# Optimization experiments

Hardware: AMD Instinct MI355X
Metric: run time of the kernel (lower is better)

## Reference

```python
import jax, jax.numpy as jnp
import numpy as np

HID = 2048      # hidden_size
NH = 32         # num query heads
NKV = 8         # num kv heads
HD = HID // NH  # head_dim = 64
E = 4           # num_experts
N = 2048        # flattened token count (divisible by E)
THETA = 10000.0
EPS = 1e-6


def setup_inputs() -> dict:
    key = jax.random.key(0)
    ks = jax.random.split(key, 8)
    s = HID ** -0.5
    return {
        "hidden_states": jax.random.normal(ks[0], (N, HID), jnp.float32),
        "positions": jnp.arange(N, dtype=jnp.int32),
        "sort_idx": jax.random.permutation(ks[1], N).astype(jnp.int32),
        "q_proj_w": jax.random.normal(ks[2], (E, HID, NH * HD), jnp.float32) * s,
        "o_proj_w": jax.random.normal(ks[3], (E, NH * HD, HID), jnp.float32) * s,
        "k_w": jax.random.normal(ks[4], (HID, NKV * HD), jnp.float32) * s,
        "v_w": jax.random.normal(ks[5], (HID, NKV * HD), jnp.float32) * s,
        "q_norm_w": jnp.ones((HD,), jnp.float32),
        "k_norm_w": jnp.ones((HD,), jnp.float32),
    }


def _routed_proj(x, weight, sort_idx):
    # x: [N, din], weight: [E, din, dout], sort_idx: permutation of N
    n, din = x.shape
    e, _, dout = weight.shape
    chunk = n // e
    sorted_x = x[sort_idx].reshape(e, chunk, din)          # gather + split
    sorted_out = jnp.einsum('ecd,edo->eco', sorted_x, weight).reshape(n, dout)
    return jnp.zeros((n, dout), sorted_out.dtype).at[sort_idx].set(sorted_out)


def _rms_norm(x, w):
    # x: [N, H, D] normalized over last dim
    var = jnp.mean(jnp.square(x), axis=-1, keepdims=True)
    return x * jax.lax.rsqrt(var + EPS) * w


def _rope_neox(x, positions):
    # x: [N, H, D]
    half = HD // 2
    inv_freq = 1.0 / (THETA ** (jnp.arange(0, HD, 2, dtype=jnp.float32) / HD))  # [D/2]
    freqs = positions.astype(jnp.float32)[:, None] * inv_freq                   # [N, D/2]
    cos = jnp.cos(freqs)[:, None, :]  # [N,1,D/2]
    sin = jnp.sin(freqs)[:, None, :]
    x1, x2 = x[..., :half], x[..., half:]
    return jnp.concatenate([x1 * cos - x2 * sin, x2 * cos + x1 * sin], axis=-1)


def reference(hidden_states, positions, sort_idx, q_proj_w, o_proj_w, k_w, v_w,
              q_norm_w, k_norm_w):
    n = hidden_states.shape[0]
    # projections
    q = _routed_proj(hidden_states, q_proj_w, sort_idx)        # [N, NH*HD]
    k = hidden_states @ k_w                                    # [N, NKV*HD]
    v = hidden_states @ v_w                                    # [N, NKV*HD]
    # qk norm per head
    q = _rms_norm(q.reshape(n, NH, HD), q_norm_w)
    k = _rms_norm(k.reshape(n, NKV, HD), k_norm_w)
    # rotary (neox style)
    q = _rope_neox(q, positions)
    k = _rope_neox(k, positions)
    v = v.reshape(n, NKV, HD)
    # GQA causal attention over the packed sequence
    g = NH // NKV
    k_rep = jnp.repeat(k, g, axis=1)  # [N, NH, HD]
    v_rep = jnp.repeat(v, g, axis=1)
    scores = jnp.einsum('qhd,khd->hqk', q, k_rep) * (HD ** -0.5)
    causal = positions[:, None] >= positions[None, :]          # [N, N]
    scores = jnp.where(causal[None], scores, jnp.finfo(scores.dtype).min)
    attn = jax.nn.softmax(scores, axis=-1)
    o = jnp.einsum('hqk,khd->qhd', attn, v_rep).reshape(n, NH * HD)
    # routed output projection
    return _routed_proj(o, o_proj_w, sort_idx)
```

## Files before the change

### kernel.cpp

```cpp
#include <hip/hip_runtime.h>
#include <hip/hip_bf16.h>

#define N_TOK 2048
#define HID   2048
#define NH    32
#define NKV   8
#define HD    64
#define NEXP  4
#define CHUNK (N_TOK / NEXP)

typedef __attribute__((ext_vector_type(8))) short short8;
typedef __attribute__((ext_vector_type(4))) short short4v;
typedef __attribute__((ext_vector_type(4))) float float4v;

#define QSCALE (0.125f * 1.44269504f)
#define RLOG   0.41524101186f

__device__ inline short f2bf(float f) {
    __hip_bfloat16 h = __float2bfloat16(f);
    return *reinterpret_cast<short*>(&h);
}
__device__ inline float bf2f(short s) {
    __hip_bfloat16 h = *reinterpret_cast<__hip_bfloat16*>(&s);
    return __bfloat162float(h);
}
__device__ __forceinline__ float fast_exp2(float x) {
    float r;
    asm("v_exp_f32 %0, %1" : "=v"(r) : "v"(x));
    return r;
}

__device__ __forceinline__ void gld_lds16(const void* g, void* l) {
    __builtin_amdgcn_global_load_lds(
        (const __attribute__((address_space(1))) unsigned int*)g,
        (__attribute__((address_space(3))) unsigned int*)l, 16, 0, 0);
}

__device__ __forceinline__ void wtrans_tile(
    const float* __restrict__ in, short* __restrict__ out, int Nw,
    int k0, int n0, float (*T)[65], int t)
{
    const int nl4 = (t & 15) * 4;
    const int kl  = t >> 4;
#pragma unroll
    for (int i = 0; i < 4; i++) {
        float4 v = *(const float4*)&in[(size_t)(k0 + kl + i * 16) * Nw + n0 + nl4];
        float* Tr = &T[kl + i * 16][nl4];
        Tr[0] = v.x; Tr[1] = v.y; Tr[2] = v.z; Tr[3] = v.w;
    }
    __syncthreads();
#pragma unroll
    for (int i = 0; i < 2; i++) {
        int idx = t + i * 256;
        int nl = idx >> 3, k8 = (idx & 7) * 8;
        short8 s;
#pragma unroll
        for (int j = 0; j < 8; j++) s[j] = f2bf(T[k8 + j][nl]);
        *(short8*)&out[(size_t)(n0 + nl) * 2048 + k0 + k8] = s;
    }
}

__global__ __launch_bounds__(256)
void prep1(const float* __restrict__ hidden, const float* __restrict__ qw,
           const float* __restrict__ kw, const float* __restrict__ vw,
           short* __restrict__ Xbf, short* __restrict__ Wq,
           short* __restrict__ Wkv)
{
    __shared__ float T[64][65];
    const int b = blockIdx.x;
    const int t = threadIdx.x;

    if (b < 2048) {
        size_t i = (size_t)b * 256 + t;
        float4 a = ((const float4*)hidden)[i * 2];
        float4 c = ((const float4*)hidden)[i * 2 + 1];
        short8 s;
        s[0] = f2bf(a.x); s[1] = f2bf(a.y); s[2] = f2bf(a.z); s[3] = f2bf(a.w);
        s[4] = f2bf(c.x); s[5] = f2bf(c.y); s[6] = f2bf(c.z); s[7] = f2bf(c.w);
        ((short8*)Xbf)[i] = s;
    } else if (b < 6144) {
        int b2 = b - 2048;
        int k0 = (b2 & 31) * 64, n0 = ((b2 >> 5) & 31) * 64, e = b2 >> 10;
        wtrans_tile(qw + (size_t)e * 2048 * 2048, Wq + (size_t)e * 2048 * 2048,
                    2048, k0, n0, T, t);
    } else {
        int b3 = b - 6144;
        int k0 = (b3 & 31) * 64, n0 = ((b3 >> 5) & 7) * 64, z = b3 >> 8;
        wtrans_tile(z ? vw : kw, Wkv + (size_t)z * 512 * 2048, 512, k0, n0, T, t);
    }
}

template <int EPI>
__device__ __forceinline__ void gemm_core(
    const short* __restrict__ X, const short* __restrict__ Wt,
    const int* __restrict__ sidx, void* __restrict__ OUT,
    int dout, bool routed, int bx, int by,
    const int* __restrict__ positions, const float* __restrict__ nw,
    short* __restrict__ vt,
    short* As0, short* Bs0, short* As1, short* Bs1, int* ridx)
{
    const int t  = threadIdx.x;
    const int m0 = by * 64;
    const int n0 = bx * 128;

    if (t < 64) ridx[t] = routed ? sidx[m0 + t] : (m0 + t);
    __syncthreads();

    const short* Wb = Wt + (routed ? (size_t)(m0 / CHUNK) * (size_t)dout * 2048 : 0);

    const int seg = (((t & 3) ^ ((t >> 3) & 3))) * 8;
    const short* ga0 = X  + (size_t)ridx[t >> 2] * 2048 + seg;
    const short* gb0 = Wb + (size_t)(n0 + (t >> 2)) * 2048 + seg;
    const short* gb1 = Wb + (size_t)(n0 + 64 + (t >> 2)) * 2048 + seg;

    const int lane = t & 63;
    const int wave = t >> 6;
    const int wl   = wave * 64 * 8;
    const int col  = lane & 15;
    const int rowg = lane >> 4;
    const int wm   = (wave >> 1) * 32;
    const int wn   = (wave & 1) * 64;

    const int swz = (col >> 1) & 3;
    int offA[2], offB[4];
#pragma unroll
    for (int i = 0; i < 2; i++)
        offA[i] = (wm + i * 16 + col) * 32 + ((rowg ^ swz) * 8);
#pragma unroll
    for (int i = 0; i < 4; i++)
        offB[i] = (wn + i * 16 + col) * 32 + ((rowg ^ swz) * 8);

    float4v acc[2][4];
#pragma unroll
    for (int mt = 0; mt < 2; mt++)
#pragma unroll
        for (int nt = 0; nt < 4; nt++) acc[mt][nt] = (float4v){0.f, 0.f, 0.f, 0.f};

    auto stage = [&](int k0, short* A, short* B) {
        gld_lds16(ga0 + k0, A + wl);
        gld_lds16(gb0 + k0, B + wl);
        gld_lds16(gb1 + k0, B + 256 * 8 + wl);
    };
    auto compute = [&](const short* A, const short* B) {
        short8 af[2], bfr[4];
#pragma unroll
        for (int i = 0; i < 2; i++) af[i] = *(const short8*)&A[offA[i]];
#pragma unroll
        for (int i = 0; i < 4; i++) bfr[i] = *(const short8*)&B[offB[i]];
#pragma unroll
        for (int mt = 0; mt < 2; mt++)
#pragma unroll
            for (int nt = 0; nt < 4; nt++)
                acc[mt][nt] = __builtin_amdgcn_mfma_f32_16x16x32_bf16(
                    af[mt], bfr[nt], acc[mt][nt], 0, 0, 0);
    };

    stage(0, As0, Bs0);
    asm volatile("s_waitcnt vmcnt(0)" ::: "memory");
    __builtin_amdgcn_s_barrier();

#pragma unroll 1
    for (int k0 = 0; k0 < 2048; k0 += 64) {
        stage(k0 + 32, As1, Bs1);
        compute(As0, Bs0);
        asm volatile("s_waitcnt vmcnt(0)" ::: "memory");
        __builtin_amdgcn_s_barrier();

        if (k0 + 64 < 2048) stage(k0 + 64, As0, Bs0);
        compute(As1, Bs1);
        asm volatile("s_waitcnt vmcnt(0)" ::: "memory");
        __builtin_amdgcn_s_barrier();
    }

    if (EPI == 0) {
#pragma unroll
        for (int mt = 0; mt < 2; mt++)
#pragma unroll
            for (int r = 0; r < 4; r++) {
                int row = ridx[wm + mt * 16 + rowg * 4 + r];
#pragma unroll
                for (int nt = 0; nt < 4; nt++)
                    ((float*)OUT)[(size_t)row * dout + n0 + wn + nt * 16 + col] =
                        acc[mt][nt][r];
            }
        return;
    }

    const bool is_v = (EPI == 2) && (n0 + wn >= 512);

    if (is_v) {
#pragma unroll
        for (int mt = 0; mt < 2; mt++) {
            int rowb = m0 + wm + mt * 16 + rowg * 4;
#pragma unroll
            for (int nt = 0; nt < 4; nt++) {
                int d = n0 + wn + nt * 16 + col - 512;
                short4v sv;
#pragma unroll
                for (int r = 0; r < 4; r++) sv[r] = f2bf(acc[mt][nt][r]);
                *(short4v*)&vt[(size_t)d * N_TOK + rowb] = sv;
            }
        }
        return;
    }

    {
        const int   h     = (n0 + wn) >> 6;
        const float oscl  = (EPI == 1) ? QSCALE : 1.0f;
        const int   ldo   = (EPI == 1) ? 2048 : 512;
        short* ob = (short*)OUT;
        float invf0 = fast_exp2(-(float)col * RLOG);
        float invf1 = fast_exp2(-(float)(16 + col) * RLOG);
        float wv[4];
#pragma unroll
        for (int nt = 0; nt < 4; nt++) wv[nt] = nw[nt * 16 + col];

#pragma unroll
        for (int mt = 0; mt < 2; mt++)
#pragma unroll
            for (int r = 0; r < 4; r++) {
                int row = ridx[wm + mt * 16 + rowg * 4 + r];
                float x0 = acc[mt][0][r], x1 = acc[mt][1][r];
                float x2 = acc[mt][2][r], x3 = acc[mt][3][r];
                float ss = x0 * x0 + x1 * x1 + x2 * x2 + x3 * x3;
#pragma unroll
                for (int off = 1; off < 16; off <<= 1)
                    ss += __shfl_xor(ss, off, 64);
                float rs = rsqrtf(ss * (1.0f / HD) + 1e-6f);
                x0 *= rs * wv[0]; x1 *= rs * wv[1];
                x2 *= rs * wv[2]; x3 *= rs * wv[3];
                float pos = (float)positions[row];
                float fr0 = pos * invf0, fr1 = pos * invf1;
                float c0 = __cosf(fr0), s0 = __sinf(fr0);
                float c1 = __cosf(fr1), s1 = __sinf(fr1);
                float o0 = x0 * c0 - x2 * s0;
                float o1 = x1 * c1 - x3 * s1;
                float o2 = x2 * c0 + x0 * s0;
                float o3 = x3 * c1 + x1 * s1;
                size_t base = (size_t)row * ldo + h * 64 + col;
                ob[base]      = f2bf(o0 * oscl);
                ob[base + 16] = f2bf(o1 * oscl);
                ob[base + 32] = f2bf(o2 * oscl);
                ob[base + 48] = f2bf(o3 * oscl);
            }
    }
}

__global__ __launch_bounds__(256)
void gemm_qkv(const short* __restrict__ X, const short* __restrict__ Wq,
              const short* __restrict__ Wkv, const int* __restrict__ sidx,
              short* __restrict__ qb, short* __restrict__ kb,
              short* __restrict__ vt, const int* __restrict__ positions,
              const float* __restrict__ qnw, const float* __restrict__ knw)
{
    __shared__ __align__(16) short As0[64 * 32], Bs0[128 * 32];
    __shared__ __align__(16) short As1[64 * 32], Bs1[128 * 32];
    __shared__ int ridx[64];
    int b = blockIdx.x;
    if (b < 512)
        gemm_core<1>(X, Wq, sidx, qb, 2048, true, b & 15, b >> 4,
                     positions, qnw, nullptr, As0, Bs0, As1, Bs1, ridx);
    else {
        b -= 512;
        gemm_core<2>(X, Wkv, nullptr, kb, 1024, false, b & 7, b >> 3,
                     positions, knw, vt, As0, Bs0, As1, Bs1, ridx);
    }
}

__global__ __launch_bounds__(256)
void gemm_o(const short* __restrict__ X, const short* __restrict__ Wt,
            const int* __restrict__ sidx, float* __restrict__ OUT)
{
    __shared__ __align__(16) short As0[64 * 32], Bs0[128 * 32];
    __shared__ __align__(16) short As1[64 * 32], Bs1[128 * 32];
    __shared__ int ridx[64];
    gemm_core<0>(X, Wt, sidx, OUT, 2048, true, blockIdx.x, blockIdx.y,
                 nullptr, nullptr, nullptr, As0, Bs0, As1, Bs1, ridx);
}

__global__ __launch_bounds__(256)
void attn_plus(const short* __restrict__ qb, const short* __restrict__ kb,
               const short* __restrict__ vt, const int* __restrict__ positions,
               short* __restrict__ ob,
               const float* __restrict__ ow, short* __restrict__ Wo)
{
    __shared__ __align__(16) char smem[27648];
    const int b = blockIdx.x;
    const int t = threadIdx.x;

    if (b >= 512) {
        float (*T)[65] = (float(*)[65])smem;
        int b2 = b - 512;
        int k0 = (b2 & 31) * 64, n0 = ((b2 >> 5) & 31) * 64, e = b2 >> 10;
        wtrans_tile(ow + (size_t)e * 2048 * 2048, Wo + (size_t)e * 2048 * 2048,
                    2048, k0, n0, T, t);
        return;
    }

    short (*Ks)[72] = (short(*)[72])smem;
    short (*Vt)[72] = (short(*)[72])(smem + 64 * 72 * 2);
    short (*Ps)[72] = (short(*)[72])(smem + 2 * 64 * 72 * 2);

    const int head = b >> 4;
    const int kvh  = head >> 2;
    const int lane = t & 63;
    const int wave = t >> 6;
    const int rowg = lane >> 4;
    const int col  = lane & 15;

    const int sr = t >> 2;
    const int sc = (t & 3) * 16;
    const float BIAS = 9.0f * 1.44269504f;

#pragma unroll
    for (int pass = 0; pass < 2; pass++) {
        const int qt = pass == 0 ? (31 - (b & 15)) : (b & 15);
        const int q0 = qt * 64;
        const int m0 = q0 + wave * 16;

        const short* qrow = qb + (size_t)(m0 + col) * HID + head * HD;
        short8 aq0 = *(const short8*)(qrow + rowg * 8);
        short8 aq1 = *(const short8*)(qrow + 32 + rowg * 8);

        int pq[4];
        float l_i[4];
#pragma unroll
        for (int r = 0; r < 4; r++) {
            pq[r] = positions[m0 + rowg * 4 + r];
            l_i[r] = 0.f;
        }
        float4v oacc[4];
#pragma unroll
        for (int n = 0; n < 4; n++) oacc[n] = (float4v){0.f, 0.f, 0.f, 0.f};

        const short* kpb = kb + (size_t)sr * 512 + kvh * HD + sc;
        const short* vpb = vt + ((size_t)kvh * HD + sr) * N_TOK + sc;

        const int nkt = qt + 1;
        short8 kA, kB, vA, vB;
        {
            kA = *(const short8*)(kpb);
            kB = *(const short8*)(kpb + 8);
            vA = *(const short8*)(vpb);
            vB = *(const short8*)(vpb + 8);
        }

        for (int kt = 0; kt < nkt; kt++) {
            __syncthreads();
            *(short8*)&Ks[sr][sc]     = kA;
            *(short8*)&Ks[sr][sc + 8] = kB;
            *(short8*)&Vt[sr][sc]     = vA;
            *(short8*)&Vt[sr][sc + 8] = vB;
            __syncthreads();

            if (kt + 1 < nkt) {
                kA = *(const short8*)(kpb + (size_t)(kt + 1) * 64 * 512);
                kB = *(const short8*)(kpb + (size_t)(kt + 1) * 64 * 512 + 8);
                vA = *(const short8*)(vpb + (kt + 1) * 64);
                vB = *(const short8*)(vpb + (kt + 1) * 64 + 8);
            }

            const int k0 = kt * 64;
            float4v c[4];
#pragma unroll
            for (int j = 0; j < 4; j++) {
                short8 blo = *(const short8*)&Ks[j * 16 + col][rowg * 8];
                short8 bhi = *(const short8*)&Ks[j * 16 + col][32 + rowg * 8];
                float4v cc = (float4v){0.f, 0.f, 0.f, 0.f};
                cc = __builtin_amdgcn_mfma_f32_16x16x32_bf16(aq0, blo, cc, 0, 0, 0);
                cc = __builtin_amdgcn_mfma_f32_16x16x32_bf16(aq1, bhi, cc, 0, 0, 0);
                c[j] = cc;
            }

            if (kt == qt) {
#pragma unroll
                for (int j = 0; j < 4; j++) {
                    int pk = positions[k0 + j * 16 + col];
#pragma unroll
                    for (int r = 0; r < 4; r++)
                        if (pq[r] < pk) c[j][r] = -1e30f;
                }
            }

#pragma unroll
            for (int j = 0; j < 4; j++)
#pragma unroll
                for (int r = 0; r < 4; r++) {
                    float p = fast_exp2(c[j][r] - BIAS);
                    l_i[r] += p;
                    Ps[wave * 16 + rowg * 4 + r][j * 16 + col] = f2bf(p);
                }

            __asm__ volatile("s_waitcnt lgkmcnt(0)" ::: "memory");

            short8 ap0 = *(const short8*)&Ps[wave * 16 + col][rowg * 8];
            short8 ap1 = *(const short8*)&Ps[wave * 16 + col][32 + rowg * 8];
#pragma unroll
            for (int n = 0; n < 4; n++) {
                short8 blo = *(const short8*)&Vt[n * 16 + col][rowg * 8];
                short8 bhi = *(const short8*)&Vt[n * 16 + col][32 + rowg * 8];
                float4v a2 = oacc[n];
                a2 = __builtin_amdgcn_mfma_f32_16x16x32_bf16(ap0, blo, a2, 0, 0, 0);
                a2 = __builtin_amdgcn_mfma_f32_16x16x32_bf16(ap1, bhi, a2, 0, 0, 0);
                oacc[n] = a2;
            }
        }

#pragma unroll
        for (int r = 0; r < 4; r++) {
#pragma unroll
            for (int off = 1; off < 16; off <<= 1)
                l_i[r] += __shfl_xor(l_i[r], off, 64);
            l_i[r] = 1.f / l_i[r];
        }
#pragma unroll
        for (int n = 0; n < 4; n++)
#pragma unroll
            for (int r = 0; r < 4; r++)
                ob[(size_t)(m0 + rowg * 4 + r) * HID + head * HD + n * 16 + col] =
                    f2bf(oacc[n][r] * l_i[r]);
    }
}

extern "C" void kernel_launch(void* const* d_in, const int* in_sizes, int n_in,
                              void* d_out, int out_size, void* d_ws, size_t ws_size,
                              hipStream_t stream)
{
    (void)in_sizes; (void)n_in; (void)out_size; (void)ws_size;

    const float* hidden    = (const float*)d_in[0];
    const int*   positions = (const int*)  d_in[1];
    const int*   sort_idx  = (const int*)  d_in[2];
    const float* q_proj_w  = (const float*)d_in[3];
    const float* o_proj_w  = (const float*)d_in[4];
    const float* k_w       = (const float*)d_in[5];
    const float* v_w       = (const float*)d_in[6];
    const float* q_norm_w  = (const float*)d_in[7];
    const float* k_norm_w  = (const float*)d_in[8];
    float* out = (float*)d_out;

    const size_t M1 = 1024 * 1024;
    short* Wqo = (short*)d_ws;
    short* Wkv = Wqo + 16 * M1;
    short* Xbf = Wkv + 2 * M1;
    short* qb  = Xbf + 4 * M1;
    short* kb  = qb  + 4 * M1;
    short* vt  = kb  + 1 * M1;
    short* obf = Xbf;

    prep1<<<6656, 256, 0, stream>>>(hidden, q_proj_w, k_w, v_w, Xbf, Wqo, Wkv);

    gemm_qkv<<<768, 256, 0, stream>>>(Xbf, Wqo, Wkv, sort_idx, qb, kb, vt,
                                      positions, q_norm_w, k_norm_w);

    attn_plus<<<4608, 256, 0, stream>>>(qb, kb, vt, positions, obf,
                                        o_proj_w, Wqo);

    gemm_o<<<dim3(16, 32), 256, 0, stream>>>(obf, Wqo, sort_idx, out);
}
```

Before: 298.5 us.

## Enlarge attention query tile to 128 rows per block, halving K/V staging

The attention blocks now process 128 query rows each (two 16-row MFMA sub-tiles per wave) instead of 64, so each staged K/V tile in shared memory is reused across twice as many queries and the number of attention blocks halves. The causal mask covers the last two key tiles, and wave priority is raised around MFMA sections. This cuts global K/V traffic and barrier count per query, at the cost of more registers per thread, a larger LDS allocation, and fewer blocks to balance the causal triangle.

```diff
diff --git a/kernel.cpp b/kernel.cpp
--- a/kernel.cpp
+++ b/kernel.cpp
@@ -284,13 +284,13 @@
                short* __restrict__ ob,
                const float* __restrict__ ow, short* __restrict__ Wo)
 {
-    __shared__ __align__(16) char smem[27648];
+    __shared__ __align__(16) char smem[36864];
     const int b = blockIdx.x;
     const int t = threadIdx.x;
 
-    if (b >= 512) {
+    if (b >= 256) {
         float (*T)[65] = (float(*)[65])smem;
-        int b2 = b - 512;
+        int b2 = b - 256;
         int k0 = (b2 & 31) * 64, n0 = ((b2 >> 5) & 31) * 64, e = b2 >> 10;
         wtrans_tile(ow + (size_t)e * 2048 * 2048, Wo + (size_t)e * 2048 * 2048,
                     2048, k0, n0, T, t);
@@ -301,7 +301,7 @@
     short (*Vt)[72] = (short(*)[72])(smem + 64 * 72 * 2);
     short (*Ps)[72] = (short(*)[72])(smem + 2 * 64 * 72 * 2);
 
-    const int head = b >> 4;
+    const int head = b >> 3;
     const int kvh  = head >> 2;
     const int lane = t & 63;
     const int wave = t >> 6;
@@ -314,29 +314,35 @@
 
 #pragma unroll
     for (int pass = 0; pass < 2; pass++) {
-        const int qt = pass == 0 ? (31 - (b & 15)) : (b & 15);
-        const int q0 = qt * 64;
-        const int m0 = q0 + wave * 16;
-
-        const short* qrow = qb + (size_t)(m0 + col) * HID + head * HD;
-        short8 aq0 = *(const short8*)(qrow + rowg * 8);
-        short8 aq1 = *(const short8*)(qrow + 32 + rowg * 8);
-
-        int pq[4];
-        float l_i[4];
-#pragma unroll
-        for (int r = 0; r < 4; r++) {
-            pq[r] = positions[m0 + rowg * 4 + r];
-            l_i[r] = 0.f;
+        const int qt = pass == 0 ? (15 - (b & 7)) : (b & 7);
+        const int q0 = qt * 128;
+        const int mw = q0 + wave * 32;
+
+        short8 aq[2][2];
+        int pq[2][4];
+        float l_i[2][4];
+#pragma unroll
+        for (int mh = 0; mh < 2; mh++) {
+            const short* qrow = qb + (size_t)(mw + mh * 16 + col) * HID + head * HD;
+            aq[mh][0] = *(const short8*)(qrow + rowg * 8);
+            aq[mh][1] = *(const short8*)(qrow + 32 + rowg * 8);
+#pragma unroll
+            for (int r = 0; r < 4; r++) {
+                pq[mh][r] = positions[mw + mh * 16 + rowg * 4 + r];
+                l_i[mh][r] = 0.f;
+            }
         }
-        float4v oacc[4];
-#pragma unroll
-        for (int n = 0; n < 4; n++) oacc[n] = (float4v){0.f, 0.f, 0.f, 0.f};
+        float4v oacc[2][4];
+#pragma unroll
+        for (int mh = 0; mh < 2; mh++)
+#pragma unroll
+            for (int n = 0; n < 4; n++) oacc[mh][n] = (float4v){0.f, 0.f, 0.f, 0.f};
 
         const short* kpb = kb + (size_t)sr * 512 + kvh * HD + sc;
         const short* vpb = vt + ((size_t)kvh * HD + sr) * N_TOK + sc;
 
-        const int nkt = qt + 1;
+        const int dq  = 2 * qt;
+        const int nkt = dq + 2;
         short8 kA, kB, vA, vB;
         {
             kA = *(const short8*)(kpb);
@@ -361,24 +367,32 @@
             }
 
             const int k0 = kt * 64;
-            float4v c[4];
+            float4v cA[4], cB[4];
+            __builtin_amdgcn_s_setprio(1);
 #pragma unroll
             for (int j = 0; j < 4; j++) {
                 short8 blo = *(const short8*)&Ks[j * 16 + col][rowg * 8];
                 short8 bhi = *(const short8*)&Ks[j * 16 + col][32 + rowg * 8];
                 float4v cc = (float4v){0.f, 0.f, 0.f, 0.f};
-                cc = __builtin_amdgcn_mfma_f32_16x16x32_bf16(aq0, blo, cc, 0, 0, 0);
-                cc = __builtin_amdgcn_mfma_f32_16x16x32_bf16(aq1, bhi, cc, 0, 0, 0);
-                c[j] = cc;
-            }
-
-            if (kt == qt) {
+                cc = __builtin_amdgcn_mfma_f32_16x16x32_bf16(aq[0][0], blo, cc, 0, 0, 0);
+                cc = __builtin_amdgcn_mfma_f32_16x16x32_bf16(aq[0][1], bhi, cc, 0, 0, 0);
+                cA[j] = cc;
+                float4v cd = (float4v){0.f, 0.f, 0.f, 0.f};
+                cd = __builtin_amdgcn_mfma_f32_16x16x32_bf16(aq[1][0], blo, cd, 0, 0, 0);
+                cd = __builtin_amdgcn_mfma_f32_16x16x32_bf16(aq[1][1], bhi, cd, 0, 0, 0);
+                cB[j] = cd;
+            }
+            __builtin_amdgcn_s_setprio(0);
+
+            if (kt >= dq) {
 #pragma unroll
                 for (int j = 0; j < 4; j++) {
                     int pk = positions[k0 + j * 16 + col];
 #pragma unroll
-                    for (int r = 0; r < 4; r++)
-                        if (pq[r] < pk) c[j][r] = -1e30f;
+                    for (int r = 0; r < 4; r++) {
+                        if (pq[0][r] < pk) cA[j][r] = -1e30f;
+                        if (pq[1][r] < pk) cB[j][r] = -1e30f;
+                    }
                 }
             }
 
@@ -386,39 +400,53 @@
             for (int j = 0; j < 4; j++)
 #pragma unroll
                 for (int r = 0; r < 4; r++) {
-                    float p = fast_exp2(c[j][r] - BIAS);
-                    l_i[r] += p;
-                    Ps[wave * 16 + rowg * 4 + r][j * 16 + col] = f2bf(p);
+                    float pa = fast_exp2(cA[j][r] - BIAS);
+                    float pb = fast_exp2(cB[j][r] - BIAS);
+                    l_i[0][r] += pa;
+                    l_i[1][r] += pb;
+                    Ps[wave * 32 + rowg * 4 + r][j * 16 + col]      = f2bf(pa);
+                    Ps[wave * 32 + 16 + rowg * 4 + r][j * 16 + col] = f2bf(pb);
                 }
 
             __asm__ volatile("s_waitcnt lgkmcnt(0)" ::: "memory");
 
-            short8 ap0 = *(const short8*)&Ps[wave * 16 + col][rowg * 8];
-            short8 ap1 = *(const short8*)&Ps[wave * 16 + col][32 + rowg * 8];
+            short8 apA0 = *(const short8*)&Ps[wave * 32 + col][rowg * 8];
+            short8 apA1 = *(const short8*)&Ps[wave * 32 + col][32 + rowg * 8];
+            short8 apB0 = *(const short8*)&Ps[wave * 32 + 16 + col][rowg * 8];
+            short8 apB1 = *(const short8*)&Ps[wave * 32 + 16 + col][32 + rowg * 8];
+            __builtin_amdgcn_s_setprio(1);
 #pragma unroll
             for (int n = 0; n < 4; n++) {
                 short8 blo = *(const short8*)&Vt[n * 16 + col][rowg * 8];
                 short8 bhi = *(const short8*)&Vt[n * 16 + col][32 + rowg * 8];
-                float4v a2 = oacc[n];
-                a2 = __builtin_amdgcn_mfma_f32_16x16x32_bf16(ap0, blo, a2, 0, 0, 0);
-                a2 = __builtin_amdgcn_mfma_f32_16x16x32_bf16(ap1, bhi, a2, 0, 0, 0);
-                oacc[n] = a2;
-            }
+                float4v a2 = oacc[0][n];
+                a2 = __builtin_amdgcn_mfma_f32_16x16x32_bf16(apA0, blo, a2, 0, 0, 0);
+                a2 = __builtin_amdgcn_mfma_f32_16x16x32_bf16(apA1, bhi, a2, 0, 0, 0);
+                oacc[0][n] = a2;
+                float4v b2 = oacc[1][n];
+                b2 = __builtin_amdgcn_mfma_f32_16x16x32_bf16(apB0, blo, b2, 0, 0, 0);
+                b2 = __builtin_amdgcn_mfma_f32_16x16x32_bf16(apB1, bhi, b2, 0, 0, 0);
+                oacc[1][n] = b2;
+            }
+            __builtin_amdgcn_s_setprio(0);
         }
 
 #pragma unroll
-        for (int r = 0; r < 4; r++) {
-#pragma unroll
-            for (int off = 1; off < 16; off <<= 1)
-                l_i[r] += __shfl_xor(l_i[r], off, 64);
-            l_i[r] = 1.f / l_i[r];
+        for (int mh = 0; mh < 2; mh++) {
+#pragma unroll
+            for (int r = 0; r < 4; r++) {
+#pragma unroll
+                for (int off = 1; off < 16; off <<= 1)
+                    l_i[mh][r] += __shfl_xor(l_i[mh][r], off, 64);
+                l_i[mh][r] = 1.f / l_i[mh][r];
+            }
+#pragma unroll
+            for (int n = 0; n < 4; n++)
+#pragma unroll
+                for (int r = 0; r < 4; r++)
+                    ob[(size_t)(mw + mh * 16 + rowg * 4 + r) * HID + head * HD +
+                       n * 16 + col] = f2bf(oacc[mh][n][r] * l_i[mh][r]);
         }
-#pragma unroll
-        for (int n = 0; n < 4; n++)
-#pragma unroll
-            for (int r = 0; r < 4; r++)
-                ob[(size_t)(m0 + rowg * 4 + r) * HID + head * HD + n * 16 + col] =
-                    f2bf(oacc[n][r] * l_i[r]);
     }
 }
 
@@ -453,7 +481,7 @@
     gemm_qkv<<<768, 256, 0, stream>>>(Xbf, Wqo, Wkv, sort_idx, qb, kb, vt,
                                       positions, q_norm_w, k_norm_w);
 
-    attn_plus<<<4608, 256, 0, stream>>>(qb, kb, vt, positions, obf,
+    attn_plus<<<4352, 256, 0, stream>>>(qb, kb, vt, positions, obf,
                                         o_proj_w, Wqo);
 
     gemm_o<<<dim3(16, 32), 256, 0, stream>>>(obf, Wqo, sort_idx, out);
```

Measured after the change: 304.5 us. +2.0%, slower.

## Load K/V fragments directly from global memory instead of staging through LDS

Applied to the files above, without the earlier changes.

The attention loop no longer stages K and V tiles through shared memory with two block barriers per tile. Each wave now reads its MFMA B-operand fragments straight from global memory (relying on L1/L2 caching), which cuts the LDS footprint and may raise occupancy. It also wraps the MFMA sections in s_setprio. The cost is redundant global loads across the four waves and no software prefetch, which exposes memory latency inside the loop.

```diff
diff --git a/kernel.cpp b/kernel.cpp
--- a/kernel.cpp
+++ b/kernel.cpp
@@ -284,7 +284,7 @@
                short* __restrict__ ob,
                const float* __restrict__ ow, short* __restrict__ Wo)
 {
-    __shared__ __align__(16) char smem[27648];
+    __shared__ __align__(16) char smem[16896];
     const int b = blockIdx.x;
     const int t = threadIdx.x;
 
@@ -297,9 +297,7 @@
         return;
     }
 
-    short (*Ks)[72] = (short(*)[72])smem;
-    short (*Vt)[72] = (short(*)[72])(smem + 64 * 72 * 2);
-    short (*Ps)[72] = (short(*)[72])(smem + 2 * 64 * 72 * 2);
+    short (*Ps)[72] = (short(*)[72])smem;
 
     const int head = b >> 4;
     const int kvh  = head >> 2;
@@ -308,9 +306,10 @@
     const int rowg = lane >> 4;
     const int col  = lane & 15;
 
-    const int sr = t >> 2;
-    const int sc = (t & 3) * 16;
     const float BIAS = 9.0f * 1.44269504f;
+
+    const short* kbase = kb + kvh * HD;
+    const short* vbase = vt + (size_t)kvh * HD * N_TOK;
 
 #pragma unroll
     for (int pass = 0; pass < 2; pass++) {
@@ -333,44 +332,25 @@
 #pragma unroll
         for (int n = 0; n < 4; n++) oacc[n] = (float4v){0.f, 0.f, 0.f, 0.f};
 
-        const short* kpb = kb + (size_t)sr * 512 + kvh * HD + sc;
-        const short* vpb = vt + ((size_t)kvh * HD + sr) * N_TOK + sc;
-
         const int nkt = qt + 1;
-        short8 kA, kB, vA, vB;
-        {
-            kA = *(const short8*)(kpb);
-            kB = *(const short8*)(kpb + 8);
-            vA = *(const short8*)(vpb);
-            vB = *(const short8*)(vpb + 8);
-        }
-
+
+#pragma unroll 1
         for (int kt = 0; kt < nkt; kt++) {
-            __syncthreads();
-            *(short8*)&Ks[sr][sc]     = kA;
-            *(short8*)&Ks[sr][sc + 8] = kB;
-            *(short8*)&Vt[sr][sc]     = vA;
-            *(short8*)&Vt[sr][sc + 8] = vB;
-            __syncthreads();
-
-            if (kt + 1 < nkt) {
-                kA = *(const short8*)(kpb + (size_t)(kt + 1) * 64 * 512);
-                kB = *(const short8*)(kpb + (size_t)(kt + 1) * 64 * 512 + 8);
-                vA = *(const short8*)(vpb + (kt + 1) * 64);
-                vB = *(const short8*)(vpb + (kt + 1) * 64 + 8);
-            }
-
             const int k0 = kt * 64;
+
             float4v c[4];
+            __builtin_amdgcn_s_setprio(1);
 #pragma unroll
             for (int j = 0; j < 4; j++) {
-                short8 blo = *(const short8*)&Ks[j * 16 + col][rowg * 8];
-                short8 bhi = *(const short8*)&Ks[j * 16 + col][32 + rowg * 8];
+                const short* kr = kbase + (size_t)(k0 + j * 16 + col) * 512;
+                short8 blo = *(const short8*)(kr + rowg * 8);
+                short8 bhi = *(const short8*)(kr + 32 + rowg * 8);
                 float4v cc = (float4v){0.f, 0.f, 0.f, 0.f};
                 cc = __builtin_amdgcn_mfma_f32_16x16x32_bf16(aq0, blo, cc, 0, 0, 0);
                 cc = __builtin_amdgcn_mfma_f32_16x16x32_bf16(aq1, bhi, cc, 0, 0, 0);
                 c[j] = cc;
             }
+            __builtin_amdgcn_s_setprio(0);
 
             if (kt == qt) {
 #pragma unroll
@@ -395,15 +375,19 @@
 
             short8 ap0 = *(const short8*)&Ps[wave * 16 + col][rowg * 8];
             short8 ap1 = *(const short8*)&Ps[wave * 16 + col][32 + rowg * 8];
+
+            __builtin_amdgcn_s_setprio(1);
 #pragma unroll
             for (int n = 0; n < 4; n++) {
-                short8 blo = *(const short8*)&Vt[n * 16 + col][rowg * 8];
-                short8 bhi = *(const short8*)&Vt[n * 16 + col][32 + rowg * 8];
+                const short* vr = vbase + (size_t)(n * 16 + col) * N_TOK + k0;
+                short8 blo = *(const short8*)(vr + rowg * 8);
+                short8 bhi = *(const short8*)(vr + 32 + rowg * 8);
                 float4v a2 = oacc[n];
                 a2 = __builtin_amdgcn_mfma_f32_16x16x32_bf16(ap0, blo, a2, 0, 0, 0);
                 a2 = __builtin_amdgcn_mfma_f32_16x16x32_bf16(ap1, bhi, a2, 0, 0, 0);
                 oacc[n] = a2;
             }
+            __builtin_amdgcn_s_setprio(0);
         }
 
 #pragma unroll
```

Result: slower. 395.1 us (+32.4%).

## Double GEMM K-tile to 64 with new LDS swizzle; raise MFMA priority in attention

Applied to the files above, without the earlier changes.

The GEMM core now stages 64-wide K slices per buffer instead of 32, with a new per-wave load mapping and an XOR swizzle over 8 segments. Each compute step runs two MFMA k-substeps, which halves the number of barriers and waitcnts per K. LDS use per GEMM block doubles, which may lower occupancy. The attention loop also wraps its MFMA sections in s_setprio so those waves are favoured during matrix work.

```diff
diff --git a/kernel.cpp b/kernel.cpp
--- a/kernel.cpp
+++ b/kernel.cpp
@@ -108,28 +108,20 @@
 
     const short* Wb = Wt + (routed ? (size_t)(m0 / CHUNK) * (size_t)dout * 2048 : 0);
 
-    const int seg = (((t & 3) ^ ((t >> 3) & 3))) * 8;
-    const short* ga0 = X  + (size_t)ridx[t >> 2] * 2048 + seg;
-    const short* gb0 = Wb + (size_t)(n0 + (t >> 2)) * 2048 + seg;
-    const short* gb1 = Wb + (size_t)(n0 + 64 + (t >> 2)) * 2048 + seg;
-
     const int lane = t & 63;
     const int wave = t >> 6;
-    const int wl   = wave * 64 * 8;
+    const int lr   = lane >> 3;
+    const int seg  = ((lane & 7) ^ lr) * 8;
+
+    const short* ga0 = X + (size_t)ridx[wave * 16 + lr] * 2048 + seg;
+    const short* ga1 = X + (size_t)ridx[wave * 16 + 8 + lr] * 2048 + seg;
+    const short* gb  = Wb + (size_t)(n0 + wave * 32 + lr) * 2048 + seg;
+
     const int col  = lane & 15;
     const int rowg = lane >> 4;
     const int wm   = (wave >> 1) * 32;
     const int wn   = (wave & 1) * 64;
 
-    const int swz = (col >> 1) & 3;
-    int offA[2], offB[4];
-#pragma unroll
-    for (int i = 0; i < 2; i++)
-        offA[i] = (wm + i * 16 + col) * 32 + ((rowg ^ swz) * 8);
-#pragma unroll
-    for (int i = 0; i < 4; i++)
-        offB[i] = (wn + i * 16 + col) * 32 + ((rowg ^ swz) * 8);
-
     float4v acc[2][4];
 #pragma unroll
     for (int mt = 0; mt < 2; mt++)
@@ -137,22 +129,31 @@
         for (int nt = 0; nt < 4; nt++) acc[mt][nt] = (float4v){0.f, 0.f, 0.f, 0.f};
 
     auto stage = [&](int k0, short* A, short* B) {
-        gld_lds16(ga0 + k0, A + wl);
-        gld_lds16(gb0 + k0, B + wl);
-        gld_lds16(gb1 + k0, B + 256 * 8 + wl);
+        gld_lds16(ga0 + k0, A + wave * 1024);
+        gld_lds16(ga1 + k0, A + wave * 1024 + 512);
+        gld_lds16(gb + k0,             B + wave * 2048);
+        gld_lds16(gb + 8 * 2048 + k0,  B + wave * 2048 + 512);
+        gld_lds16(gb + 16 * 2048 + k0, B + wave * 2048 + 1024);
+        gld_lds16(gb + 24 * 2048 + k0, B + wave * 2048 + 1536);
     };
     auto compute = [&](const short* A, const short* B) {
-        short8 af[2], bfr[4];
-#pragma unroll
-        for (int i = 0; i < 2; i++) af[i] = *(const short8*)&A[offA[i]];
-#pragma unroll
-        for (int i = 0; i < 4; i++) bfr[i] = *(const short8*)&B[offB[i]];
-#pragma unroll
-        for (int mt = 0; mt < 2; mt++)
-#pragma unroll
-            for (int nt = 0; nt < 4; nt++)
-                acc[mt][nt] = __builtin_amdgcn_mfma_f32_16x16x32_bf16(
-                    af[mt], bfr[nt], acc[mt][nt], 0, 0, 0);
+#pragma unroll
+        for (int kk = 0; kk < 2; kk++) {
+            const int sl = (((kk * 4 + rowg) ^ (col & 7))) * 8;
+            short8 af[2], bfr[4];
+#pragma unroll
+            for (int i = 0; i < 2; i++)
+                af[i] = *(const short8*)&A[(wm + i * 16 + col) * 64 + sl];
+#pragma unroll
+            for (int i = 0; i < 4; i++)
+                bfr[i] = *(const short8*)&B[(wn + i * 16 + col) * 64 + sl];
+#pragma unroll
+            for (int mt = 0; mt < 2; mt++)
+#pragma unroll
+                for (int nt = 0; nt < 4; nt++)
+                    acc[mt][nt] = __builtin_amdgcn_mfma_f32_16x16x32_bf16(
+                        af[mt], bfr[nt], acc[mt][nt], 0, 0, 0);
+        }
     };
 
     stage(0, As0, Bs0);
@@ -160,13 +161,13 @@
     __builtin_amdgcn_s_barrier();
 
 #pragma unroll 1
-    for (int k0 = 0; k0 < 2048; k0 += 64) {
-        stage(k0 + 32, As1, Bs1);
+    for (int k0 = 0; k0 < 2048; k0 += 128) {
+        if (k0 + 64 < 2048) stage(k0 + 64, As1, Bs1);
         compute(As0, Bs0);
         asm volatile("s_waitcnt vmcnt(0)" ::: "memory");
         __builtin_amdgcn_s_barrier();
 
-        if (k0 + 64 < 2048) stage(k0 + 64, As0, Bs0);
+        if (k0 + 128 < 2048) stage(k0 + 128, As0, Bs0);
         compute(As1, Bs1);
         asm volatile("s_waitcnt vmcnt(0)" ::: "memory");
         __builtin_amdgcn_s_barrier();
@@ -253,8 +254,8 @@
               short* __restrict__ vt, const int* __restrict__ positions,
               const float* __restrict__ qnw, const float* __restrict__ knw)
 {
-    __shared__ __align__(16) short As0[64 * 32], Bs0[128 * 32];
-    __shared__ __align__(16) short As1[64 * 32], Bs1[128 * 32];
+    __shared__ __align__(16) short As0[64 * 64], Bs0[128 * 64];
+    __shared__ __align__(16) short As1[64 * 64], Bs1[128 * 64];
     __shared__ int ridx[64];
     int b = blockIdx.x;
     if (b < 512)
@@ -271,8 +272,8 @@
 void gemm_o(const short* __restrict__ X, const short* __restrict__ Wt,
             const int* __restrict__ sidx, float* __restrict__ OUT)
 {
-    __shared__ __align__(16) short As0[64 * 32], Bs0[128 * 32];
-    __shared__ __align__(16) short As1[64 * 32], Bs1[128 * 32];
+    __shared__ __align__(16) short As0[64 * 64], Bs0[128 * 64];
+    __shared__ __align__(16) short As1[64 * 64], Bs1[128 * 64];
     __shared__ int ridx[64];
     gemm_core<0>(X, Wt, sidx, OUT, 2048, true, blockIdx.x, blockIdx.y,
                  nullptr, nullptr, nullptr, As0, Bs0, As1, Bs1, ridx);
@@ -362,6 +363,7 @@
 
             const int k0 = kt * 64;
             float4v c[4];
+            __builtin_amdgcn_s_setprio(1);
 #pragma unroll
             for (int j = 0; j < 4; j++) {
                 short8 blo = *(const short8*)&Ks[j * 16 + col][rowg * 8];
@@ -371,6 +373,7 @@
                 cc = __builtin_amdgcn_mfma_f32_16x16x32_bf16(aq1, bhi, cc, 0, 0, 0);
                 c[j] = cc;
             }
+            __builtin_amdgcn_s_setprio(0);
 
             if (kt == qt) {
 #pragma unroll
@@ -395,6 +398,7 @@
 
             short8 ap0 = *(const short8*)&Ps[wave * 16 + col][rowg * 8];
             short8 ap1 = *(const short8*)&Ps[wave * 16 + col][32 + rowg * 8];
+            __builtin_amdgcn_s_setprio(1);
 #pragma unroll
             for (int n = 0; n < 4; n++) {
                 short8 blo = *(const short8*)&Vt[n * 16 + col][rowg * 8];
@@ -404,6 +408,7 @@
                 a2 = __builtin_amdgcn_mfma_f32_16x16x32_bf16(ap1, bhi, a2, 0, 0, 0);
                 oacc[n] = a2;
             }
+            __builtin_amdgcn_s_setprio(0);
         }
 
 #pragma unroll
```

Measured after the change: 270.1 us. 1.1x faster.
